# Kernel tuning notes

Measured on AMD Instinct MI355X. Metric: run time of the kernel, lower is better.

Reference implementation:

```python
import jax, jax.numpy as jnp
import numpy as np
import math

B, N, NRES = 2, 1024, 256
CS, CCOND, CZ, H = 256, 384, 64, 8
DH = CS // H
INF = 1e5


def _ln(x, g=None, b=None, eps=1e-5):
    mu = jnp.mean(x, axis=-1, keepdims=True)
    var = jnp.mean((x - mu) ** 2, axis=-1, keepdims=True)
    y = (x - mu) * jax.lax.rsqrt(var + eps)
    if g is not None:
        y = y * g
    if b is not None:
        y = y + b
    return y


def setup_inputs() -> dict:
    key = jax.random.key(0)
    ks = jax.random.split(key, 20)
    w = lambda k, sh: (jax.random.normal(k, sh, jnp.float32) * 0.02)
    return {
        "s": jax.random.normal(ks[0], (B, NRES, CCOND), jnp.float32),
        "rigids_embed": jax.random.normal(ks[1], (B, N, CS), jnp.float32),
        "framepair_embed": jax.random.normal(ks[2], (B, N, N, CZ), jnp.float32),
        "rigids_mask": jnp.ones((B, N), jnp.float32),
        "rigids_to_res_idx": jax.random.randint(ks[3], (B, N), 0, NRES, jnp.int64 if jax.config.jax_enable_x64 else jnp.int32),
        # attention params
        "ln_g": jnp.ones((CS,), jnp.float32), "ln_b": jnp.zeros((CS,), jnp.float32),
        "Wq": w(ks[4], (CS, CS)), "Wkv": w(ks[5], (CS, 2 * CS)),
        "lnz_g": jnp.ones((CZ,), jnp.float32), "lnz_b": jnp.zeros((CZ,), jnp.float32),
        "Wbias": w(ks[6], (CZ, H)), "Wg": w(ks[7], (CS, CS)), "Wo": w(ks[8], (CS, CS)),
        # transition / AdaLN params
        "lncond_g": jnp.ones((CCOND,), jnp.float32),
        "Wc1": w(ks[9], (CCOND, CS)), "bc1": jnp.zeros((CS,), jnp.float32),
        "Wcn": w(ks[10], (CCOND, CS)),
        "W1": w(ks[11], (CS, 2 * CS)), "W2": w(ks[12], (CS, 2 * CS)),
        "Wc2": w(ks[13], (CCOND, CS)), "bc2": jnp.full((CS,), -2.0, jnp.float32),
        "Wb": w(ks[14], (2 * CS, CS)),
    }


def reference(s, rigids_embed, framepair_embed, rigids_mask, rigids_to_res_idx,
              ln_g, ln_b, Wq, Wkv, lnz_g, lnz_b, Wbias, Wg, Wo,
              lncond_g, Wc1, bc1, Wcn, W1, W2, Wc2, bc2, Wb):
    b_, n_, _ = rigids_embed.shape
    # ---- BlockAttentionPairBias (to_queries/to_keys = identity) ----
    edge_mask = rigids_mask[:, :, None] * rigids_mask[:, None, :]          # [B,N,N]
    x = _ln(rigids_embed, ln_g, ln_b)                                      # [B,N,CS]
    q = (x @ Wq).reshape(b_, n_, H, DH)
    kv = (x @ Wkv).reshape(b_, n_, 2 * H, DH)
    k, v = kv[:, :, :H], kv[:, :, H:]
    a = jnp.einsum('bihd,bjhd->bhij', q, k) / math.sqrt(DH)                # [B,H,N,N]
    pb = _ln(framepair_embed, lnz_g, lnz_b) @ Wbias                        # [B,N,N,H]
    a = a + jnp.transpose(pb, (0, 3, 1, 2))
    a = a + (edge_mask - 1.0)[:, None, :, :] * INF
    a = jax.nn.softmax(a, axis=-1)
    o = jnp.einsum('bhij,bjhd->bihd', a, v).reshape(b_, n_, CS)
    gate = jax.nn.sigmoid(x @ Wg)
    update = (o * gate) @ Wo
    rig = rigids_embed + update * rigids_mask[..., None]

    # ---- GatherConditionedTransition ----
    idx = rigids_to_res_idx[..., None]                                     # [B,N,1]
    sn = _ln(rig)                                                          # no affine
    cn = _ln(s, lncond_g)                                                  # weight, no bias
    cond_gate = jnp.take_along_axis(cn @ Wc1 + bc1, idx, axis=1) * rigids_mask[..., None]
    cond_bias = jnp.take_along_axis(cn @ Wcn, idx, axis=1) * rigids_mask[..., None]
    sa = sn * jax.nn.sigmoid(cond_gate) + cond_bias
    bmid = jax.nn.silu(sa @ W1) * (sa @ W2)                                # [B,N,2CS]
    cg = jnp.take_along_axis(s @ Wc2 + bc2, idx, axis=1) * rigids_mask[..., None]
    tout = jax.nn.sigmoid(cg) * (bmid @ Wb)
    return rig + tout * rigids_mask[..., None]
```

## Files before the change

kernel.cpp:

```cpp
#include <hip/hip_runtime.h>
#include <math.h>

#define DEVI __device__ __forceinline__
typedef float fv4 __attribute__((ext_vector_type(4)));
typedef float f32x4 __attribute__((ext_vector_type(4)));
typedef short bf16x8 __attribute__((ext_vector_type(8)));
typedef unsigned short us4 __attribute__((ext_vector_type(4)));

DEVI float sigm(float x){ return 1.f/(1.f+__expf(-x)); }
DEVI unsigned short f2bf(float f){
    unsigned int u = __float_as_uint(f);
    u = (u + 0x7FFFu + ((u >> 16) & 1u)) >> 16;
    return (unsigned short)u;
}
DEVI float bf2f(unsigned short u){ return __uint_as_float(((unsigned int)u)<<16); }

DEVI void blockReduce2(float& s1, float& s2, float* red){
    #pragma unroll
    for (int m=1;m<64;m<<=1){ s1+=__shfl_xor(s1,m); s2+=__shfl_xor(s2,m); }
    const int w = threadIdx.x>>6;
    if ((threadIdx.x&63)==0){ red[w]=s1; red[8+w]=s2; }
    __syncthreads();
    s1 = red[0]+red[1]+red[2]+red[3];
    s2 = red[8]+red[9]+red[10]+red[11];
}

__global__ __launch_bounds__(256) void ln_rows(const float* __restrict__ in,
                                               const float* __restrict__ g,
                                               const float* __restrict__ bt,
                                               float* __restrict__ out, int C){
    __shared__ float red[16];
    const size_t row = blockIdx.x;
    const float* x = in + row*(size_t)C;
    float s1=0.f, s2=0.f;
    for (int c=threadIdx.x; c<C; c+=256){ float v=x[c]; s1+=v; s2+=v*v; }
    blockReduce2(s1,s2,red);
    const float inv = 1.f/(float)C;
    const float mu = s1*inv;
    const float rs = rsqrtf(s2*inv - mu*mu + 1e-5f);
    float* o = out + row*(size_t)C;
    for (int c=threadIdx.x; c<C; c+=256){
        float y = (x[c]-mu)*rs;
        if (g)  y *= g[c];
        if (bt) y += bt[c];
        o[c] = y;
    }
}

__global__ __launch_bounds__(256) void ln_rows_bf(const float* __restrict__ in,
                                                  const float* __restrict__ g,
                                                  const float* __restrict__ bt,
                                                  unsigned short* __restrict__ out){
    __shared__ float red[16];
    const size_t row = blockIdx.x;
    const int t = threadIdx.x;
    const float v = in[row*256 + t];
    float s1=v, s2=v*v;
    blockReduce2(s1,s2,red);
    const float mu = s1*(1.f/256.f);
    const float rs = rsqrtf(s2*(1.f/256.f) - mu*mu + 1e-5f);
    out[row*256 + t] = f2bf((v-mu)*rs*g[t] + bt[t]);
}

__global__ __launch_bounds__(256) void cast_all(
    const float* __restrict__ Wq, const float* __restrict__ Wkv,
    const float* __restrict__ Wg, const float* __restrict__ Wo,
    const float* __restrict__ W1, const float* __restrict__ W2,
    const float* __restrict__ Wb,
    unsigned short* __restrict__ wcatT, unsigned short* __restrict__ WoT,
    unsigned short* __restrict__ W1T, unsigned short* __restrict__ W2T,
    unsigned short* __restrict__ WbT)
{
    __shared__ unsigned short tile[64][65];
    const int z = blockIdx.z;
    const float* src; unsigned short* dst; int K, N;
    switch(z){
      case 0: src=Wq;  dst=wcatT;           K=256; N=256; break;
      case 1: src=Wkv; dst=wcatT+256*256;   K=256; N=512; break;
      case 2: src=Wg;  dst=wcatT+768*256;   K=256; N=256; break;
      case 3: src=Wo;  dst=WoT;             K=256; N=256; break;
      case 4: src=W1;  dst=W1T;             K=256; N=512; break;
      case 5: src=W2;  dst=W2T;             K=256; N=512; break;
      default: src=Wb; dst=WbT;             K=512; N=256; break;
    }
    const int nt = blockIdx.x*64, kt = blockIdx.y*64;
    if (nt >= N || kt >= K) return;
    const int t = threadIdx.x;
    const int c = t & 63, r0 = t >> 6;
    #pragma unroll 4
    for (int rr=r0; rr<64; rr+=4)
        tile[rr][c] = f2bf(src[(size_t)(kt+rr)*N + nt + c]);
    __syncthreads();
    #pragma unroll 4
    for (int rr=r0; rr<64; rr+=4)
        dst[(size_t)(nt+rr)*K + kt + c] = tile[c][rr];
}

__global__ __launch_bounds__(256) void vtrans(const unsigned short* __restrict__ qkvbf,
                                              unsigned short* __restrict__ vTb){
    __shared__ unsigned short tile[64][65];
    const int t = threadIdx.x;
    const int jt = blockIdx.x*64, dt = blockIdx.y*64, bz = blockIdx.z;
    const int c = t & 63, r0 = t >> 6;
    #pragma unroll 4
    for (int rr=r0; rr<64; rr+=4)
        tile[rr][c] = qkvbf[(size_t)((bz<<10)+jt+rr)*1024 + 512 + dt + c];
    __syncthreads();
    #pragma unroll 4
    for (int rr=r0; rr<64; rr+=4)
        vTb[((size_t)(bz*256 + dt + rr))*1024 + jt + c] = tile[c][rr];
}

template<int MODE>
__global__ __launch_bounds__(256) void mfma_gemm(
    const unsigned short* __restrict__ A, int lda,
    const unsigned short* __restrict__ Bt, int ldbt,
    float* __restrict__ C, int ldc,
    int K,
    const float* __restrict__ resid,
    const float* __restrict__ mask,
    const float* __restrict__ gsrc,
    const int* __restrict__ idxp)
{
    __shared__ unsigned short As[64*40];
    __shared__ unsigned short Bs[64*40];
    const int t = threadIdx.x;
    const int lane = t & 63, wave = t >> 6;
    const int wr = wave >> 1, wc = wave & 1;
    const int bm = blockIdx.x*64, bn = blockIdx.y*64;
    const int srow = t >> 2, sk = (t & 3) * 8;
    const int l15 = lane & 15, lk = (lane >> 4) * 8;
    f32x4 acc[2][2] = {};
    for (int kt = 0; kt < K; kt += 32){
        *(uint4*)&As[srow*40 + sk] = *(const uint4*)&A [(size_t)(bm+srow)*lda  + kt + sk];
        *(uint4*)&Bs[srow*40 + sk] = *(const uint4*)&Bt[(size_t)(bn+srow)*ldbt + kt + sk];
        __syncthreads();
        bf16x8 a0 = *(const bf16x8*)&As[(32*wr +  0 + l15)*40 + lk];
        bf16x8 a1 = *(const bf16x8*)&As[(32*wr + 16 + l15)*40 + lk];
        bf16x8 b0 = *(const bf16x8*)&Bs[(32*wc +  0 + l15)*40 + lk];
        bf16x8 b1 = *(const bf16x8*)&Bs[(32*wc + 16 + l15)*40 + lk];
        acc[0][0] = __builtin_amdgcn_mfma_f32_16x16x32_bf16(a0,b0,acc[0][0],0,0,0);
        acc[0][1] = __builtin_amdgcn_mfma_f32_16x16x32_bf16(a0,b1,acc[0][1],0,0,0);
        acc[1][0] = __builtin_amdgcn_mfma_f32_16x16x32_bf16(a1,b0,acc[1][0],0,0,0);
        acc[1][1] = __builtin_amdgcn_mfma_f32_16x16x32_bf16(a1,b1,acc[1][1],0,0,0);
        __syncthreads();
    }
    const int rbase = (lane >> 4) * 4;
    #pragma unroll
    for (int m=0;m<2;++m){
        #pragma unroll
        for (int r=0;r<4;++r){
            const int grow = bm + 32*wr + 16*m + rbase + r;
            #pragma unroll
            for (int n=0;n<2;++n){
                const int gcol = bn + 32*wc + 16*n + l15;
                float v = acc[m][n][r];
                if (MODE==1){
                    const float mi = mask[grow];
                    C[(size_t)grow*ldc + gcol] = resid[(size_t)grow*256 + gcol] + v*mi;
                } else {
                    const float mi = mask[grow];
                    const int id = idxp[grow];
                    const int bbi = grow >> 10;
                    const float cg = gsrc[((size_t)(bbi*256+id))*256 + gcol]*mi;
                    C[(size_t)grow*ldc + gcol] = resid[(size_t)grow*256 + gcol] + sigm(cg)*v*mi;
                }
            }
        }
    }
}

__global__ __launch_bounds__(256) void mfma_gemm_bfout(
    const unsigned short* __restrict__ A, int lda,
    const unsigned short* __restrict__ Bt, int ldbt,
    unsigned short* __restrict__ C, int ldc,
    int K)
{
    __shared__ unsigned short As[64*40];
    __shared__ unsigned short Bs[64*40];
    const int t = threadIdx.x;
    const int lane = t & 63, wave = t >> 6;
    const int wr = wave >> 1, wc = wave & 1;
    const int bm = blockIdx.x*64, bn = blockIdx.y*64;
    const int srow = t >> 2, sk = (t & 3) * 8;
    const int l15 = lane & 15, lk = (lane >> 4) * 8;
    f32x4 acc[2][2] = {};
    for (int kt = 0; kt < K; kt += 32){
        *(uint4*)&As[srow*40 + sk] = *(const uint4*)&A [(size_t)(bm+srow)*lda  + kt + sk];
        *(uint4*)&Bs[srow*40 + sk] = *(const uint4*)&Bt[(size_t)(bn+srow)*ldbt + kt + sk];
        __syncthreads();
        bf16x8 a0 = *(const bf16x8*)&As[(32*wr +  0 + l15)*40 + lk];
        bf16x8 a1 = *(const bf16x8*)&As[(32*wr + 16 + l15)*40 + lk];
        bf16x8 b0 = *(const bf16x8*)&Bs[(32*wc +  0 + l15)*40 + lk];
        bf16x8 b1 = *(const bf16x8*)&Bs[(32*wc + 16 + l15)*40 + lk];
        acc[0][0] = __builtin_amdgcn_mfma_f32_16x16x32_bf16(a0,b0,acc[0][0],0,0,0);
        acc[0][1] = __builtin_amdgcn_mfma_f32_16x16x32_bf16(a0,b1,acc[0][1],0,0,0);
        acc[1][0] = __builtin_amdgcn_mfma_f32_16x16x32_bf16(a1,b0,acc[1][0],0,0,0);
        acc[1][1] = __builtin_amdgcn_mfma_f32_16x16x32_bf16(a1,b1,acc[1][1],0,0,0);
        __syncthreads();
    }
    const int rbase = (lane >> 4) * 4;
    #pragma unroll
    for (int m=0;m<2;++m){
        #pragma unroll
        for (int r=0;r<4;++r){
            const int grow = bm + 32*wr + 16*m + rbase + r;
            #pragma unroll
            for (int n=0;n<2;++n){
                const int gcol = bn + 32*wc + 16*n + l15;
                C[(size_t)grow*ldc + gcol] = f2bf(acc[m][n][r]);
            }
        }
    }
}

__global__ __launch_bounds__(256) void mfma_dual(
    const unsigned short* __restrict__ A, int lda,
    const unsigned short* __restrict__ B1t,
    const unsigned short* __restrict__ B2t, int ldbt,
    unsigned short* __restrict__ C, int ldc,
    int K)
{
    __shared__ unsigned short As[64*40];
    __shared__ unsigned short B1s[64*40];
    __shared__ unsigned short B2s[64*40];
    const int t = threadIdx.x;
    const int lane = t & 63, wave = t >> 6;
    const int wr = wave >> 1, wc = wave & 1;
    const int bm = blockIdx.x*64, bn = blockIdx.y*64;
    const int srow = t >> 2, sk = (t & 3) * 8;
    const int l15 = lane & 15, lk = (lane >> 4) * 8;
    f32x4 acc1[2][2] = {};
    f32x4 acc2[2][2] = {};
    for (int kt = 0; kt < K; kt += 32){
        *(uint4*)&As [srow*40 + sk] = *(const uint4*)&A  [(size_t)(bm+srow)*lda  + kt + sk];
        *(uint4*)&B1s[srow*40 + sk] = *(const uint4*)&B1t[(size_t)(bn+srow)*ldbt + kt + sk];
        *(uint4*)&B2s[srow*40 + sk] = *(const uint4*)&B2t[(size_t)(bn+srow)*ldbt + kt + sk];
        __syncthreads();
        bf16x8 a0 = *(const bf16x8*)&As[(32*wr +  0 + l15)*40 + lk];
        bf16x8 a1 = *(const bf16x8*)&As[(32*wr + 16 + l15)*40 + lk];
        bf16x8 p0 = *(const bf16x8*)&B1s[(32*wc +  0 + l15)*40 + lk];
        bf16x8 p1 = *(const bf16x8*)&B1s[(32*wc + 16 + l15)*40 + lk];
        bf16x8 q0 = *(const bf16x8*)&B2s[(32*wc +  0 + l15)*40 + lk];
        bf16x8 q1 = *(const bf16x8*)&B2s[(32*wc + 16 + l15)*40 + lk];
        acc1[0][0] = __builtin_amdgcn_mfma_f32_16x16x32_bf16(a0,p0,acc1[0][0],0,0,0);
        acc1[0][1] = __builtin_amdgcn_mfma_f32_16x16x32_bf16(a0,p1,acc1[0][1],0,0,0);
        acc1[1][0] = __builtin_amdgcn_mfma_f32_16x16x32_bf16(a1,p0,acc1[1][0],0,0,0);
        acc1[1][1] = __builtin_amdgcn_mfma_f32_16x16x32_bf16(a1,p1,acc1[1][1],0,0,0);
        acc2[0][0] = __builtin_amdgcn_mfma_f32_16x16x32_bf16(a0,q0,acc2[0][0],0,0,0);
        acc2[0][1] = __builtin_amdgcn_mfma_f32_16x16x32_bf16(a0,q1,acc2[0][1],0,0,0);
        acc2[1][0] = __builtin_amdgcn_mfma_f32_16x16x32_bf16(a1,q0,acc2[1][0],0,0,0);
        acc2[1][1] = __builtin_amdgcn_mfma_f32_16x16x32_bf16(a1,q1,acc2[1][1],0,0,0);
        __syncthreads();
    }
    const int rbase = (lane >> 4) * 4;
    #pragma unroll
    for (int m=0;m<2;++m){
        #pragma unroll
        for (int r=0;r<4;++r){
            const int grow = bm + 32*wr + 16*m + rbase + r;
            #pragma unroll
            for (int n=0;n<2;++n){
                const int gcol = bn + 32*wc + 16*n + l15;
                const float u1 = acc1[m][n][r];
                C[(size_t)grow*ldc + gcol] = f2bf(u1*sigm(u1)*acc2[m][n][r]);
            }
        }
    }
}

__global__ __launch_bounds__(256) void s_gemm(
    const unsigned short* __restrict__ qkvbf,
    unsigned short* __restrict__ Sb)
{
    __shared__ unsigned short As[64*40];
    __shared__ unsigned short Bs[64*40];
    const int t = threadIdx.x;
    const int lane = t & 63, wave = t >> 6;
    const int wr = wave >> 1, wc = wave & 1;
    const int bm = blockIdx.x*64, bn = blockIdx.y*64;
    const int bh = blockIdx.z, b = bh >> 3, h = bh & 7;
    const int srow = t >> 2, sk = (t & 3) * 8;
    const int l15 = lane & 15, lk = (lane >> 4) * 8;
    const unsigned short* Aq = qkvbf + (size_t)b*1024*1024 + h*32;
    const unsigned short* Bk = qkvbf + (size_t)b*1024*1024 + 256 + h*32;
    *(uint4*)&As[srow*40 + sk] = *(const uint4*)&Aq[(size_t)(bm+srow)*1024 + sk];
    *(uint4*)&Bs[srow*40 + sk] = *(const uint4*)&Bk[(size_t)(bn+srow)*1024 + sk];
    __syncthreads();
    bf16x8 a0 = *(const bf16x8*)&As[(32*wr +  0 + l15)*40 + lk];
    bf16x8 a1 = *(const bf16x8*)&As[(32*wr + 16 + l15)*40 + lk];
    bf16x8 b0 = *(const bf16x8*)&Bs[(32*wc +  0 + l15)*40 + lk];
    bf16x8 b1 = *(const bf16x8*)&Bs[(32*wc + 16 + l15)*40 + lk];
    f32x4 acc[2][2] = {};
    acc[0][0] = __builtin_amdgcn_mfma_f32_16x16x32_bf16(a0,b0,acc[0][0],0,0,0);
    acc[0][1] = __builtin_amdgcn_mfma_f32_16x16x32_bf16(a0,b1,acc[0][1],0,0,0);
    acc[1][0] = __builtin_amdgcn_mfma_f32_16x16x32_bf16(a1,b0,acc[1][0],0,0,0);
    acc[1][1] = __builtin_amdgcn_mfma_f32_16x16x32_bf16(a1,b1,acc[1][1],0,0,0);
    const float scale = 0.17677669529663687f;
    const int rbase = (lane >> 4) * 4;
    #pragma unroll
    for (int m=0;m<2;++m){
        #pragma unroll
        for (int r=0;r<4;++r){
            const int grow = bm + 32*wr + 16*m + rbase + r;
            #pragma unroll
            for (int n=0;n<2;++n){
                const int gcol = bn + 32*wc + 16*n + l15;
                const size_t idx = ((size_t)bh*1024 + grow)*1024 + gcol;
                Sb[idx] = f2bf(acc[m][n][r]*scale + bf2f(Sb[idx]));
            }
        }
    }
}

__global__ __launch_bounds__(256) void softmax_rows(unsigned short* __restrict__ S){
    __shared__ float red[16];
    const int t = threadIdx.x;
    unsigned short* base = S + (size_t)blockIdx.x*1024;
    const us4 v = *(const us4*)&base[t*4];
    float f0=bf2f(v.x), f1=bf2f(v.y), f2=bf2f(v.z), f3=bf2f(v.w);
    float m = fmaxf(fmaxf(f0,f1), fmaxf(f2,f3));
    #pragma unroll
    for (int o=1;o<64;o<<=1) m = fmaxf(m, __shfl_xor(m,o));
    const int w = t>>6;
    if ((t&63)==0) red[w] = m;
    __syncthreads();
    m = fmaxf(fmaxf(red[0],red[1]), fmaxf(red[2],red[3]));
    f0=__expf(f0-m); f1=__expf(f1-m); f2=__expf(f2-m); f3=__expf(f3-m);
    float s = f0+f1+f2+f3;
    #pragma unroll
    for (int o=1;o<64;o<<=1) s += __shfl_xor(s,o);
    if ((t&63)==0) red[8+w] = s;
    __syncthreads();
    const float inv = 1.f/(red[8]+red[9]+red[10]+red[11]);
    us4 o4;
    o4.x=f2bf(f0*inv); o4.y=f2bf(f1*inv); o4.z=f2bf(f2*inv); o4.w=f2bf(f3*inv);
    *(us4*)&base[t*4] = o4;
}

__global__ __launch_bounds__(256) void pv_gemm(
    const unsigned short* __restrict__ P,
    const unsigned short* __restrict__ vTb,
    const unsigned short* __restrict__ qkvbf,
    unsigned short* __restrict__ og)
{
    __shared__ unsigned short As[64*40];
    __shared__ unsigned short Bs[32*40];
    const int t = threadIdx.x;
    const int lane = t & 63, wave = t >> 6;
    const int bm = blockIdx.x*64;
    const int bh = blockIdx.z, b = bh >> 3, h = bh & 7;
    const int l15 = lane & 15, lk = (lane >> 4) * 8;
    const unsigned short* Pb = P   + ((size_t)bh*1024)*1024;
    const unsigned short* Vb = vTb + ((size_t)(b*256 + h*32))*1024;
    const int srow = t >> 2, sk = (t & 3) * 8;
    uint4 pfA = *(const uint4*)&Pb[(size_t)(bm+srow)*1024 + sk];
    uint4 pfB;
    if (t < 128) pfB = *(const uint4*)&Vb[(size_t)srow*1024 + sk];
    f32x4 acc0 = {}, acc1 = {};
    for (int kt = 0; kt < 1024; kt += 32){
        __syncthreads();
        *(uint4*)&As[srow*40 + sk] = pfA;
        if (t < 128) *(uint4*)&Bs[srow*40 + sk] = pfB;
        if (kt + 32 < 1024){
            pfA = *(const uint4*)&Pb[(size_t)(bm+srow)*1024 + kt + 32 + sk];
            if (t < 128) pfB = *(const uint4*)&Vb[(size_t)srow*1024 + kt + 32 + sk];
        }
        __syncthreads();
        bf16x8 a  = *(const bf16x8*)&As[(16*wave + l15)*40 + lk];
        bf16x8 b0 = *(const bf16x8*)&Bs[( 0 + l15)*40 + lk];
        bf16x8 b1 = *(const bf16x8*)&Bs[(16 + l15)*40 + lk];
        acc0 = __builtin_amdgcn_mfma_f32_16x16x32_bf16(a,b0,acc0,0,0,0);
        acc1 = __builtin_amdgcn_mfma_f32_16x16x32_bf16(a,b1,acc1,0,0,0);
    }
    const int rbase = (lane >> 4) * 4;
    #pragma unroll
    for (int r=0;r<4;++r){
        const int irow = bm + 16*wave + rbase + r;
        const size_t grow = (size_t)b*1024 + irow;
        {
            const int d = 0 + l15;
            const float gate = bf2f(qkvbf[grow*1024 + 768 + h*32 + d]);
            og[grow*256 + h*32 + d] = f2bf(acc0[r]*sigm(gate));
        }
        {
            const int d = 16 + l15;
            const float gate = bf2f(qkvbf[grow*1024 + 768 + h*32 + d]);
            og[grow*256 + h*32 + d] = f2bf(acc1[r]*sigm(gate));
        }
    }
}

__global__ __launch_bounds__(256) void gemm3(
    const float* __restrict__ cn, const float* __restrict__ s_,
    const float* __restrict__ Wc1, const float* __restrict__ Wcn,
    const float* __restrict__ Wc2,
    const float* __restrict__ bc1, const float* __restrict__ bc2,
    float* __restrict__ c1res, float* __restrict__ cbres,
    float* __restrict__ cgres)
{
    const int z = blockIdx.z;
    const float* A    = (z==2) ? s_  : cn;
    const float* B    = (z==0) ? Wc1 : (z==1) ? Wcn : Wc2;
    const float* bias = (z==0) ? bc1 : (z==2) ? bc2 : nullptr;
    float* C          = (z==0) ? c1res : (z==1) ? cbres : cgres;
    const int lda = 384, ldb = 256, ldc = 256, K = 384;
    __shared__ float As[16][68];
    __shared__ float Bs[16][68];
    const int t = threadIdx.x;
    const int tx = t & 15, ty = t >> 4;
    const int bm = blockIdx.x * 64, bn = blockIdx.y * 64;
    const int am = t >> 2, akq = (t & 3) * 4;
    const int bk = t >> 4, bnq = (t & 15) * 4;
    float acc[4][4] = {};
    for (int kt = 0; kt < K; kt += 16) {
        const float4 va = *(const float4*)&A[(size_t)(bm+am)*lda + kt + akq];
        const float4 vb = *(const float4*)&B[(size_t)(kt+bk)*ldb + bn + bnq];
        As[akq+0][am]=va.x; As[akq+1][am]=va.y; As[akq+2][am]=va.z; As[akq+3][am]=va.w;
        *(float4*)&Bs[bk][bnq] = vb;
        __syncthreads();
        #pragma unroll
        for (int kk=0; kk<16; ++kk){
            const float4 af = *(const float4*)&As[kk][ty*4];
            const float4 bf = *(const float4*)&Bs[kk][tx*4];
            acc[0][0]+=af.x*bf.x; acc[0][1]+=af.x*bf.y; acc[0][2]+=af.x*bf.z; acc[0][3]+=af.x*bf.w;
            acc[1][0]+=af.y*bf.x; acc[1][1]+=af.y*bf.y; acc[1][2]+=af.y*bf.z; acc[1][3]+=af.y*bf.w;
            acc[2][0]+=af.z*bf.x; acc[2][1]+=af.z*bf.y; acc[2][2]+=af.z*bf.z; acc[2][3]+=af.z*bf.w;
            acc[3][0]+=af.w*bf.x; acc[3][1]+=af.w*bf.y; acc[3][2]+=af.w*bf.z; acc[3][3]+=af.w*bf.w;
        }
        __syncthreads();
    }
    #pragma unroll
    for (int i=0;i<4;++i){
        const int m = bm + ty*4 + i;
        #pragma unroll
        for (int jj=0;jj<4;++jj){
            const int n = bn + tx*4 + jj;
            float v = acc[i][jj];
            if (bias) v += bias[n];
            C[(size_t)m*ldc+n] = v;
        }
    }
}

__global__ __launch_bounds__(256,6) void pb_kernel(
    const float* __restrict__ fp,
    const float* __restrict__ lnzg, const float* __restrict__ lnzb,
    const float* __restrict__ wbias,
    const float* __restrict__ mask,
    unsigned short* __restrict__ pb)
{
    __shared__ unsigned short S[8][1040];
    __shared__ float maskS[1024];
    const int t = threadIdx.x;
    const int bi = blockIdx.x;
    const int b = bi >> 10, i = bi & 1023;
    const int l = t & 15, grp = t >> 4;

    float wg[4], wb_[4];
    fv4 w0[4], w1[4];
    #pragma unroll
    for (int cc=0; cc<4; ++cc){
        const int c = 4*l + cc;
        wg[cc] = lnzg[c]; wb_[cc] = lnzb[c];
        w0[cc] = *(const fv4*)&wbias[c*8];
        w1[cc] = *(const fv4*)&wbias[c*8+4];
    }
    *(fv4*)&maskS[t*4] = ((const fv4*)(mask + (b<<10)))[t];
    __syncthreads();
    const float mi = mask[bi];

    const fv4* fpv = (const fv4*)(fp + (size_t)bi*65536);
    fv4 c0 = fpv[(size_t)grp*16 + l];
    fv4 c1 = fpv[(size_t)(grp+16)*16 + l];
    #pragma unroll 1
    for (int jt=0; jt<1024; jt+=32){
        const fv4 f0=c0, f1=c1;
        if (jt+32 < 1024){
            c0 = fpv[(size_t)(jt+32+grp)*16 + l];
            c1 = fpv[(size_t)(jt+48+grp)*16 + l];
        }
        #pragma unroll
        for (int half=0; half<2; ++half){
            const fv4 f = half ? f1 : f0;
            const int j = jt + 16*half + grp;
            float s1 = f.x+f.y+f.z+f.w;
            float s2 = f.x*f.x+f.y*f.y+f.z*f.z+f.w*f.w;
            #pragma unroll
            for (int m=1;m<16;m<<=1){ s1 += __shfl_xor(s1,m); s2 += __shfl_xor(s2,m); }
            const float mu = s1*(1.f/64.f);
            const float rs = rsqrtf(s2*(1.f/64.f) - mu*mu + 1e-5f);
            float lnv[4];
            lnv[0]=(f.x-mu)*rs*wg[0]+wb_[0];
            lnv[1]=(f.y-mu)*rs*wg[1]+wb_[1];
            lnv[2]=(f.z-mu)*rs*wg[2]+wb_[2];
            lnv[3]=(f.w-mu)*rs*wg[3]+wb_[3];
            float pv[8] = {};
            #pragma unroll
            for (int cc=0;cc<4;++cc){
                pv[0]+=lnv[cc]*w0[cc].x; pv[1]+=lnv[cc]*w0[cc].y;
                pv[2]+=lnv[cc]*w0[cc].z; pv[3]+=lnv[cc]*w0[cc].w;
                pv[4]+=lnv[cc]*w1[cc].x; pv[5]+=lnv[cc]*w1[cc].y;
                pv[6]+=lnv[cc]*w1[cc].z; pv[7]+=lnv[cc]*w1[cc].w;
            }
            {
                const bool b8 = (l & 8);
                #pragma unroll
                for (int k=0;k<4;++k){
                    const float a = b8 ? pv[k] : pv[k+4];
                    const float r = __shfl_xor(a, 8);
                    pv[k] = (b8 ? pv[k+4] : pv[k]) + r;
                }
                const bool b4 = (l & 4);
                #pragma unroll
                for (int k=0;k<2;++k){
                    const float a = b4 ? pv[k] : pv[k+2];
                    const float r = __shfl_xor(a, 4);
                    pv[k] = (b4 ? pv[k+2] : pv[k]) + r;
                }
                const bool b2 = (l & 2);
                {
                    const float a = b2 ? pv[0] : pv[1];
                    const float r = __shfl_xor(a, 2);
                    pv[0] = (b2 ? pv[1] : pv[0]) + r;
                }
                pv[0] += __shfl_xor(pv[0], 1);
            }
            if ((l & 1) == 0){
                const float mterm = (mi*maskS[j]-1.f)*100000.f;
                S[(l>>1)][j] = f2bf(pv[0] + mterm);
            }
        }
    }
    __syncthreads();
    #pragma unroll 1
    for (int k=0;k<8;++k){
        const int j4 = (t & 255) * 4;
        const us4 v = *(const us4*)&S[k][j4];
        *(us4*)&pb[(((size_t)(b*8+k))*1024 + i)*1024 + j4] = v;
    }
}

__global__ __launch_bounds__(256) void sa_kernel(
    const float* __restrict__ rig,
    const float* __restrict__ c1res,
    const float* __restrict__ cbres,
    const int* __restrict__ idxp,
    const float* __restrict__ mask,
    unsigned short* __restrict__ sa)
{
    __shared__ float red[16];
    const int m = blockIdx.x;
    const int t = threadIdx.x;
    const float v = rig[(size_t)m*256 + t];
    float s1 = v, s2 = v*v;
    blockReduce2(s1,s2,red);
    const float mu = s1*(1.f/256.f);
    const float rs = rsqrtf(s2*(1.f/256.f) - mu*mu + 1e-5f);
    const float sn = (v-mu)*rs;
    const float mi = mask[m];
    const int id = idxp[m];
    const int b = m >> 10;
    const size_t go = ((size_t)(b*256+id))*256 + t;
    const float cgate = c1res[go]*mi;
    const float cb    = cbres[go]*mi;
    sa[(size_t)m*256+t] = f2bf(sn*sigm(cgate) + cb);
}

extern "C" void kernel_launch(void* const* d_in, const int* in_sizes, int n_in,
                              void* d_out, int out_size, void* d_ws, size_t ws_size,
                              hipStream_t stream)
{
    (void)in_sizes; (void)n_in; (void)out_size; (void)ws_size;
    const float* s_     = (const float*)d_in[0];
    const float* rigids = (const float*)d_in[1];
    const float* fp     = (const float*)d_in[2];
    const float* maskp  = (const float*)d_in[3];
    const int*   idxp   = (const int*)d_in[4];
    const float* ln_g   = (const float*)d_in[5];
    const float* ln_b   = (const float*)d_in[6];
    const float* Wq     = (const float*)d_in[7];
    const float* Wkv    = (const float*)d_in[8];
    const float* lnz_g  = (const float*)d_in[9];
    const float* lnz_b  = (const float*)d_in[10];
    const float* Wbias  = (const float*)d_in[11];
    const float* Wg     = (const float*)d_in[12];
    const float* Wo     = (const float*)d_in[13];
    const float* lncond = (const float*)d_in[14];
    const float* Wc1    = (const float*)d_in[15];
    const float* bc1    = (const float*)d_in[16];
    const float* Wcn    = (const float*)d_in[17];
    const float* W1     = (const float*)d_in[18];
    const float* W2     = (const float*)d_in[19];
    const float* Wc2    = (const float*)d_in[20];
    const float* bc2    = (const float*)d_in[21];
    const float* Wb     = (const float*)d_in[22];
    float* out = (float*)d_out;

    float* ws    = (float*)d_ws;
    float* rig   = ws;
    float* cn    = rig   + 524288;
    float* c1res = cn    + 196608;
    float* cbres = c1res + 131072;
    float* cgres = cbres + 131072;
    float* bend  = cgres + 131072;
    unsigned short* xbf    = (unsigned short*)bend;
    unsigned short* ogbf   = xbf    + 524288;
    unsigned short* sabf   = ogbf   + 524288;
    unsigned short* bmidbf = sabf   + 524288;
    unsigned short* wcatT  = bmidbf + 1048576;
    unsigned short* WoT    = wcatT  + 262144;
    unsigned short* W1T    = WoT    + 65536;
    unsigned short* W2T    = W1T    + 131072;
    unsigned short* WbT    = W2T    + 131072;
    unsigned short* qkvbf  = WbT    + 131072;
    unsigned short* vTb    = qkvbf  + 2097152;
    unsigned short* pbbf   = vTb    + 524288;

    pb_kernel<<<2048,256,0,stream>>>(fp, lnz_g, lnz_b, Wbias, maskp, pbbf);
    cast_all<<<dim3(8,8,7),256,0,stream>>>(Wq, Wkv, Wg, Wo, W1, W2, Wb,
                                           wcatT, WoT, W1T, W2T, WbT);
    ln_rows_bf<<<2048,256,0,stream>>>(rigids, ln_g, ln_b, xbf);
    mfma_gemm_bfout<<<dim3(32,16),256,0,stream>>>(xbf,256, wcatT,256, qkvbf,1024, 256);
    vtrans<<<dim3(16,4,2),256,0,stream>>>(qkvbf, vTb);
    s_gemm<<<dim3(16,16,16),256,0,stream>>>(qkvbf, pbbf);
    softmax_rows<<<16384,256,0,stream>>>(pbbf);
    pv_gemm<<<dim3(16,1,16),256,0,stream>>>(pbbf, vTb, qkvbf, ogbf);
    mfma_gemm<1><<<dim3(32,4),256,0,stream>>>(ogbf,256, WoT,256, rig,256, 256, rigids, maskp, nullptr,nullptr);
    ln_rows<<<512,256,0,stream>>>(s_, lncond, nullptr, cn, 384);
    gemm3<<<dim3(8,4,3),256,0,stream>>>(cn, s_, Wc1, Wcn, Wc2, bc1, bc2, c1res, cbres, cgres);
    sa_kernel<<<2048,256,0,stream>>>(rig, c1res, cbres, idxp, maskp, sabf);
    mfma_dual<<<dim3(32,8),256,0,stream>>>(sabf,256, W1T, W2T,256, bmidbf,512, 256);
    mfma_gemm<2><<<dim3(32,4),256,0,stream>>>(bmidbf,512, WbT,512, out,256, 512, rig, maskp, cgres, idxp);
}
```

Before: 244.1 us.

## Double K-tile depth in PV GEMM and deepen framepair prefetch

The PV GEMM now stages 64-wide K tiles instead of 32, with two 16-byte global loads per thread and four MFMAs per barrier pair. This halves the number of loop iterations and __syncthreads calls. The pair-bias kernel's framepair register prefetch goes from one stage to two, putting more loads in flight to hide HBM latency. The cost is more shared memory and registers per block, which may lower occupancy.

```diff
diff --git a/kernel.cpp b/kernel.cpp
--- a/kernel.cpp
+++ b/kernel.cpp
@@ -344,8 +344,8 @@
     const unsigned short* __restrict__ qkvbf,
     unsigned short* __restrict__ og)
 {
-    __shared__ unsigned short As[64*40];
-    __shared__ unsigned short Bs[32*40];
+    __shared__ unsigned short As[64*72];
+    __shared__ unsigned short Bs[32*72];
     const int t = threadIdx.x;
     const int lane = t & 63, wave = t >> 6;
     const int bm = blockIdx.x*64;
@@ -353,25 +353,42 @@
     const int l15 = lane & 15, lk = (lane >> 4) * 8;
     const unsigned short* Pb = P   + ((size_t)bh*1024)*1024;
     const unsigned short* Vb = vTb + ((size_t)(b*256 + h*32))*1024;
-    const int srow = t >> 2, sk = (t & 3) * 8;
-    uint4 pfA = *(const uint4*)&Pb[(size_t)(bm+srow)*1024 + sk];
-    uint4 pfB;
-    if (t < 128) pfB = *(const uint4*)&Vb[(size_t)srow*1024 + sk];
+    const int srow = t >> 2, sk = (t & 3) * 16;
+    uint4 pfA0 = *(const uint4*)&Pb[(size_t)(bm+srow)*1024 + sk];
+    uint4 pfA1 = *(const uint4*)&Pb[(size_t)(bm+srow)*1024 + sk + 8];
+    uint4 pfB0, pfB1;
+    if (t < 128){
+        pfB0 = *(const uint4*)&Vb[(size_t)srow*1024 + sk];
+        pfB1 = *(const uint4*)&Vb[(size_t)srow*1024 + sk + 8];
+    }
     f32x4 acc0 = {}, acc1 = {};
-    for (int kt = 0; kt < 1024; kt += 32){
-        __syncthreads();
-        *(uint4*)&As[srow*40 + sk] = pfA;
-        if (t < 128) *(uint4*)&Bs[srow*40 + sk] = pfB;
-        if (kt + 32 < 1024){
-            pfA = *(const uint4*)&Pb[(size_t)(bm+srow)*1024 + kt + 32 + sk];
-            if (t < 128) pfB = *(const uint4*)&Vb[(size_t)srow*1024 + kt + 32 + sk];
-        }
-        __syncthreads();
-        bf16x8 a  = *(const bf16x8*)&As[(16*wave + l15)*40 + lk];
-        bf16x8 b0 = *(const bf16x8*)&Bs[( 0 + l15)*40 + lk];
-        bf16x8 b1 = *(const bf16x8*)&Bs[(16 + l15)*40 + lk];
-        acc0 = __builtin_amdgcn_mfma_f32_16x16x32_bf16(a,b0,acc0,0,0,0);
-        acc1 = __builtin_amdgcn_mfma_f32_16x16x32_bf16(a,b1,acc1,0,0,0);
+    for (int kt = 0; kt < 1024; kt += 64){
+        __syncthreads();
+        *(uint4*)&As[srow*72 + sk]     = pfA0;
+        *(uint4*)&As[srow*72 + sk + 8] = pfA1;
+        if (t < 128){
+            *(uint4*)&Bs[srow*72 + sk]     = pfB0;
+            *(uint4*)&Bs[srow*72 + sk + 8] = pfB1;
+        }
+        if (kt + 64 < 1024){
+            pfA0 = *(const uint4*)&Pb[(size_t)(bm+srow)*1024 + kt+64 + sk];
+            pfA1 = *(const uint4*)&Pb[(size_t)(bm+srow)*1024 + kt+64 + sk + 8];
+            if (t < 128){
+                pfB0 = *(const uint4*)&Vb[(size_t)srow*1024 + kt+64 + sk];
+                pfB1 = *(const uint4*)&Vb[(size_t)srow*1024 + kt+64 + sk + 8];
+            }
+        }
+        __syncthreads();
+        bf16x8 a0  = *(const bf16x8*)&As[(16*wave + l15)*72 + lk];
+        bf16x8 a1  = *(const bf16x8*)&As[(16*wave + l15)*72 + 32 + lk];
+        bf16x8 b0  = *(const bf16x8*)&Bs[( 0 + l15)*72 + lk];
+        bf16x8 b1  = *(const bf16x8*)&Bs[(16 + l15)*72 + lk];
+        bf16x8 b0h = *(const bf16x8*)&Bs[( 0 + l15)*72 + 32 + lk];
+        bf16x8 b1h = *(const bf16x8*)&Bs[(16 + l15)*72 + 32 + lk];
+        acc0 = __builtin_amdgcn_mfma_f32_16x16x32_bf16(a0,b0 ,acc0,0,0,0);
+        acc1 = __builtin_amdgcn_mfma_f32_16x16x32_bf16(a0,b1 ,acc1,0,0,0);
+        acc0 = __builtin_amdgcn_mfma_f32_16x16x32_bf16(a1,b0h,acc0,0,0,0);
+        acc1 = __builtin_amdgcn_mfma_f32_16x16x32_bf16(a1,b1h,acc1,0,0,0);
     }
     const int rbase = (lane >> 4) * 4;
     #pragma unroll
@@ -471,14 +488,17 @@
     const float mi = mask[bi];
 
     const fv4* fpv = (const fv4*)(fp + (size_t)bi*65536);
-    fv4 c0 = fpv[(size_t)grp*16 + l];
+    fv4 c0 = fpv[(size_t)(grp+ 0)*16 + l];
     fv4 c1 = fpv[(size_t)(grp+16)*16 + l];
+    fv4 c2 = fpv[(size_t)(grp+32)*16 + l];
+    fv4 c3 = fpv[(size_t)(grp+48)*16 + l];
     #pragma unroll 1
     for (int jt=0; jt<1024; jt+=32){
         const fv4 f0=c0, f1=c1;
-        if (jt+32 < 1024){
-            c0 = fpv[(size_t)(jt+32+grp)*16 + l];
-            c1 = fpv[(size_t)(jt+48+grp)*16 + l];
+        c0 = c2; c1 = c3;
+        if (jt+64 < 1024){
+            c2 = fpv[(size_t)(jt+64+grp)*16 + l];
+            c3 = fpv[(size_t)(jt+80+grp)*16 + l];
         }
         #pragma unroll
         for (int half=0; half<2; ++half){
```

Result: slower. 274.6 us (+12.5%).
